# Kernel tuning notes

Measured on AMD Instinct MI355X. Metric: run time of the kernel, lower is better.

Reference implementation:

```python
import jax, jax.numpy as jnp
import numpy as np

N_EMBD = 1024
HEAD_SIZE = 128
B, T = 8, 4096


def setup_inputs() -> dict:
    key = jax.random.key(0)
    ks = jax.random.split(key, 7)
    s = 1.0 / np.sqrt(N_EMBD)
    return {
        "x": jax.random.normal(ks[0], (B, T, N_EMBD), dtype=jnp.float32),
        "Wq": jax.random.uniform(ks[1], (N_EMBD, HEAD_SIZE), jnp.float32, -s, s),
        "bq": jax.random.uniform(ks[2], (HEAD_SIZE,), jnp.float32, -s, s),
        "Wk": jax.random.uniform(ks[3], (N_EMBD, HEAD_SIZE), jnp.float32, -s, s),
        "bk": jax.random.uniform(ks[4], (HEAD_SIZE,), jnp.float32, -s, s),
        "Wv": jax.random.uniform(ks[5], (N_EMBD, HEAD_SIZE), jnp.float32, -s, s),
        "bv": jax.random.uniform(ks[6], (HEAD_SIZE,), jnp.float32, -s, s),
    }


def reference(x, Wq, bq, Wk, bk, Wv, bv):
    # q,k,v: [B,T,H]
    q = x @ Wq + bq
    k = x @ Wk + bk
    v = x @ Wv + bv
    scale = HEAD_SIZE ** -0.5
    att = jnp.einsum("bth,bsh->bts", q, k) * scale  # [B,T,T]
    t = x.shape[1]
    causal = jnp.tril(jnp.ones((t, t), dtype=bool))
    att = jnp.where(causal, att, -jnp.inf)
    att = jax.nn.softmax(att, axis=-1)
    # dropout with p=0.0 is identity (eval-mode equivalent)
    out = jnp.einsum("bts,bsh->bth", att, v)  # [B,T,H]
    return out
```

## Files before the change

### kernel.cpp

```cpp
#include <hip/hip_runtime.h>
#include <hip/hip_bf16.h>
#include <stdint.h>

#define BATCH 8
#define SEQ   4096
#define EMB   1024
#define HD    128
#define NROWS 32768

typedef __attribute__((ext_vector_type(8))) short short8;
typedef __attribute__((ext_vector_type(4))) float f32x4;

__device__ inline unsigned short f2bf(float f) {
    union { float f; unsigned int u; } c; c.f = f;
    unsigned int u = c.u;
    unsigned int r = (u + 0x7fffu + ((u >> 16) & 1u)) >> 16;
    return (unsigned short)r;
}
__device__ inline float bf2f(unsigned short u) {
    union { unsigned int i; float f; } c; c.i = ((unsigned int)u) << 16; return c.f;
}
__device__ inline unsigned int pkbf(float a, float b) {
    __hip_bfloat162 h = __float22bfloat162_rn(make_float2(a, b));
    union { __hip_bfloat162 h; unsigned int u; } c; c.h = h; return c.u;
}

#define GLDS16(gp, lp) __builtin_amdgcn_global_load_lds( \
    (const __attribute__((address_space(1))) void*)(gp), \
    (__attribute__((address_space(3))) void*)(lp), 16, 0, 0)

__global__ __launch_bounds__(256) void prep_kernel(
    const float* __restrict__ Wq, const float* __restrict__ bq,
    const float* __restrict__ Wk, const float* __restrict__ bk,
    const float* __restrict__ Wv, const float* __restrict__ bv,
    unsigned short* __restrict__ wt, float* __restrict__ biasc)
{
    const int n = blockIdx.x;
    const int sel = n >> 7, h = n & 127;
    const float* W = (sel == 0) ? Wq : (sel == 1) ? Wk : Wv;
    const int tid = threadIdx.x;
    const int k0 = tid * 4;
    union { unsigned short us[4]; uint2 v; } pk;
#pragma unroll
    for (int u = 0; u < 4; ++u) pk.us[u] = f2bf(W[(size_t)(k0 + u) * HD + h]);
    *(uint2*)&wt[(size_t)n * EMB + k0] = pk.v;
    if (tid == 0) {
        const float* bp = (sel == 0) ? bq : (sel == 1) ? bk : bv;
        biasc[n] = bp[h];
    }
}

__global__ __launch_bounds__(512, 4) void gemm_qkv(
    const float* __restrict__ x, const unsigned short* __restrict__ wt,
    const float* __restrict__ biasc,
    unsigned short* __restrict__ q, unsigned short* __restrict__ kOut,
    unsigned short* __restrict__ vt)
{
    const int m0  = blockIdx.x * 64;
    const int tid = threadIdx.x;
    const int wave = tid >> 6, lane = tid & 63;
    const int quad = lane >> 4, l15 = lane & 15;

    __shared__ __align__(16) unsigned short As[2][64][40];
    __shared__ __align__(16) unsigned short Bs[2][12288];

    f32x4 acc[3][4];
#pragma unroll
    for (int i = 0; i < 3; ++i)
#pragma unroll
        for (int j = 0; j < 4; ++j) acc[i][j] = (f32x4){0.f, 0.f, 0.f, 0.f};

    const int arow = tid >> 3, akc = (tid & 7) * 4;
    float4 aR;

#define LOAD_A(kt) aR = *(const float4*)(x + (size_t)(m0 + arow) * EMB + (kt) * 32 + akc);
#define WRITE_A(buf)                                                        \
    {                                                                       \
        union { unsigned short us[4]; uint2 v; } pw;                        \
        pw.us[0] = f2bf(aR.x); pw.us[1] = f2bf(aR.y);                       \
        pw.us[2] = f2bf(aR.z); pw.us[3] = f2bf(aR.w);                       \
        *(uint2*)&As[buf][arow][akc] = pw.v;                                \
    }
#define STAGE_B(kt, buf)                                                    \
    {                                                                       \
        _Pragma("unroll")                                                   \
        for (int g = 0; g < 3; ++g) {                                       \
            int s0 = (g * 8 + wave) * 64;                                   \
            int s  = s0 + lane;                                             \
            int n  = s >> 2, c = (s & 3) ^ (n & 3);                         \
            GLDS16(wt + (size_t)n * EMB + (kt) * 32 + c * 8,                \
                   &Bs[buf][s0 * 8]);                                       \
        }                                                                   \
    }

    LOAD_A(0); STAGE_B(0, 0); WRITE_A(0);
    int cur = 0;

    for (int kt = 0; kt < 32; ++kt) {
        __syncthreads();
        if (kt < 31) { LOAD_A(kt + 1); STAGE_B(kt + 1, cur ^ 1); }
        short8 af[4], bw[3];
#pragma unroll
        for (int mj = 0; mj < 4; ++mj)
            af[mj] = *(const short8*)&As[cur][mj * 16 + l15][quad * 8];
#pragma unroll
        for (int ni = 0; ni < 3; ++ni) {
            int n = wave * 48 + ni * 16 + l15;
            bw[ni] = *(const short8*)&Bs[cur][n * 32 + ((quad ^ (n & 3)) << 3)];
        }
#pragma unroll
        for (int ni = 0; ni < 3; ++ni)
#pragma unroll
            for (int mj = 0; mj < 4; ++mj)
                acc[ni][mj] = __builtin_amdgcn_mfma_f32_16x16x32_bf16(
                    bw[ni], af[mj], acc[ni][mj], 0, 0, 0);
        if (kt < 31) WRITE_A(cur ^ 1);
        cur ^= 1;
    }

    const float qscale = 0.08838834764831845f * 1.4426950408889634f;
    const int bb = m0 >> 12;
    const int t0 = m0 & 4095;
#pragma unroll
    for (int ni = 0; ni < 3; ++ni) {
        int colbase = wave * 48 + ni * 16;
        int sel = colbase >> 7;
        int c0 = colbase + quad * 4;
        float4 bv4 = *(const float4*)&biasc[c0];
#pragma unroll
        for (int mj = 0; mj < 4; ++mj) {
            int m = m0 + mj * 16 + l15;
            if (sel == 0) {
                union { unsigned short us[4]; uint2 v; } pk;
#pragma unroll
                for (int j = 0; j < 4; ++j)
                    pk.us[j] = f2bf((acc[ni][mj][j] + ((const float*)&bv4)[j]) * qscale);
                *(uint2*)&q[(size_t)m * HD + (c0 & 127)] = pk.v;
            } else if (sel == 1) {
                union { unsigned short us[4]; uint2 v; } pk;
#pragma unroll
                for (int j = 0; j < 4; ++j)
                    pk.us[j] = f2bf(acc[ni][mj][j] + ((const float*)&bv4)[j]);
                *(uint2*)&kOut[(size_t)m * HD + (c0 & 127)] = pk.v;
            } else {
#pragma unroll
                for (int j = 0; j < 4; ++j) {
                    int h = (c0 & 127) + j;
                    vt[((size_t)(bb * 128 + h)) * SEQ + t0 + mj * 16 + l15] =
                        f2bf(acc[ni][mj][j] + ((const float*)&bv4)[j]);
                }
            }
        }
    }
#undef LOAD_A
#undef WRITE_A
#undef STAGE_B
}

__global__ __launch_bounds__(512, 2) void attn_kernel(
    const unsigned short* __restrict__ q, const unsigned short* __restrict__ k,
    const unsigned short* __restrict__ vt, float* __restrict__ outA,
    unsigned short* __restrict__ Oh, float2* __restrict__ ml)
{
    const int rank   = blockIdx.x;
    const int qtA    = 31 - (rank >> 4);
    const int parity = (rank >> 3) & 1;
    const int b      = rank & 7;
    const int tid  = threadIdx.x;
    const int wave = tid >> 6, lane = tid & 63;
    const int quad = lane >> 4, l15 = lane & 15;
    const int qtW   = (wave < 4) ? qtA : (31 - qtA);
    const int qrow0 = qtW * 128 + (wave & 3) * 32;
    const size_t qbase = (size_t)b * SEQ;
    const size_t vbase = (size_t)b * HD * SEQ;

    __shared__ __align__(16) unsigned short Ks[2][8192];
    __shared__ __align__(16) unsigned short Vs[2][8192];

#define STAGE_KV(kt_, buf_)                                                  \
    {                                                                        \
        _Pragma("unroll")                                                    \
        for (int g = 0; g < 2; ++g) {                                        \
            int s0 = (g * 8 + wave) * 64;                                    \
            int s  = s0 + lane;                                              \
            int key = s >> 4, c = (s & 15) ^ (key & 15);                     \
            GLDS16(k + (qbase + (kt_) * 64 + key) * HD + c * 8,              \
                   &Ks[buf_][s0 * 8]);                                       \
        }                                                                    \
        _Pragma("unroll")                                                    \
        for (int g = 0; g < 2; ++g) {                                        \
            int s0 = (g * 8 + wave) * 64;                                    \
            int s  = s0 + lane;                                              \
            int h = s >> 3, c = (s & 7) ^ (h & 7);                           \
            GLDS16(vt + vbase + (size_t)h * SEQ + (kt_) * 64 + c * 8,        \
                   &Vs[buf_][s0 * 8]);                                       \
        }                                                                    \
    }

    short8 qf[2][4];
#pragma unroll
    for (int mi = 0; mi < 2; ++mi)
#pragma unroll
        for (int kh = 0; kh < 4; ++kh)
            qf[mi][kh] = *(const short8*)(q + (qbase + qrow0 + mi * 16 + l15) * HD + kh * 32 + quad * 8);

    f32x4 o[2][8];
#pragma unroll
    for (int mi = 0; mi < 2; ++mi)
#pragma unroll
        for (int hi = 0; hi < 8; ++hi) o[mi][hi] = (f32x4){0.f, 0.f, 0.f, 0.f};
    float m_r[2] = {-1e30f, -1e30f};
    float l_r[2] = {0.f, 0.f};

    const int bpa0 = (l15 + 16 * ((2 * quad) & 3)) * 4;
    const int bpa1 = (l15 + 16 * ((2 * quad + 1) & 3)) * 4;

    const int niter = qtA + 1;
    STAGE_KV(parity, 0);
    int cur = 0;

    for (int i = 0; i < niter; ++i) {
        const int kt = parity + 2 * i;
        const int key0 = kt * 64;
        __syncthreads();
        if (i + 1 < niter) STAGE_KV(kt + 2, cur ^ 1);

        if (i <= qtW) {
            f32x4 s[2][4];
#pragma unroll
            for (int mi = 0; mi < 2; ++mi)
#pragma unroll
                for (int ni = 0; ni < 4; ++ni) s[mi][ni] = (f32x4){0.f, 0.f, 0.f, 0.f};
#pragma unroll
            for (int kh = 0; kh < 4; ++kh) {
#pragma unroll
                for (int ni = 0; ni < 4; ++ni) {
                    short8 kf = *(const short8*)&Ks[cur][(ni * 16 + l15) * 128 + (((kh * 4 + quad) ^ l15) << 3)];
                    s[0][ni] = __builtin_amdgcn_mfma_f32_16x16x32_bf16(kf, qf[0][kh], s[0][ni], 0, 0, 0);
                    s[1][ni] = __builtin_amdgcn_mfma_f32_16x16x32_bf16(kf, qf[1][kh], s[1][ni], 0, 0, 0);
                }
            }
            if (key0 + 63 > qrow0) {
#pragma unroll
                for (int mi = 0; mi < 2; ++mi)
#pragma unroll
                    for (int ni = 0; ni < 4; ++ni)
#pragma unroll
                        for (int j = 0; j < 4; ++j) {
                            int key = key0 + ni * 16 + quad * 4 + j;
                            int t   = qrow0 + mi * 16 + l15;
                            if (key > t) s[mi][ni][j] = -1e30f;
                        }
            }
            unsigned int pk[2][4][2];
#pragma unroll
            for (int mi = 0; mi < 2; ++mi) {
                float mx = -1e30f;
#pragma unroll
                for (int ni = 0; ni < 4; ++ni)
#pragma unroll
                    for (int j = 0; j < 4; ++j) mx = fmaxf(mx, s[mi][ni][j]);
                mx = fmaxf(mx, __shfl_xor(mx, 16));
                mx = fmaxf(mx, __shfl_xor(mx, 32));
                float mnew = fmaxf(m_r[mi], mx);
                float alpha = __builtin_amdgcn_exp2f(m_r[mi] - mnew);
                m_r[mi] = mnew;
                float rs = 0.f;
#pragma unroll
                for (int ni = 0; ni < 4; ++ni) {
                    float p0 = __builtin_amdgcn_exp2f(s[mi][ni][0] - mnew);
                    float p1 = __builtin_amdgcn_exp2f(s[mi][ni][1] - mnew);
                    float p2 = __builtin_amdgcn_exp2f(s[mi][ni][2] - mnew);
                    float p3 = __builtin_amdgcn_exp2f(s[mi][ni][3] - mnew);
                    rs += (p0 + p1) + (p2 + p3);
                    pk[mi][ni][0] = pkbf(p0, p1);
                    pk[mi][ni][1] = pkbf(p2, p3);
                }
                rs += __shfl_xor(rs, 16);
                rs += __shfl_xor(rs, 32);
                l_r[mi] = alpha * l_r[mi] + rs;
#pragma unroll
                for (int hi = 0; hi < 8; ++hi) o[mi][hi] *= alpha;
            }
            short8 pT[2][2];
#pragma unroll
            for (int mi = 0; mi < 2; ++mi)
#pragma unroll
                for (int sk = 0; sk < 2; ++sk) {
                    union { unsigned int u[4]; short8 s8; } pt;
                    int lo = 2 * sk, hi_ = 2 * sk + 1;
                    unsigned int a0 = (unsigned)__builtin_amdgcn_ds_bpermute(bpa0, (int)pk[mi][lo][0]);
                    unsigned int b0 = (unsigned)__builtin_amdgcn_ds_bpermute(bpa0, (int)pk[mi][hi_][0]);
                    pt.u[0] = (quad < 2) ? a0 : b0;
                    unsigned int a1 = (unsigned)__builtin_amdgcn_ds_bpermute(bpa0, (int)pk[mi][lo][1]);
                    unsigned int b1 = (unsigned)__builtin_amdgcn_ds_bpermute(bpa0, (int)pk[mi][hi_][1]);
                    pt.u[1] = (quad < 2) ? a1 : b1;
                    unsigned int a2 = (unsigned)__builtin_amdgcn_ds_bpermute(bpa1, (int)pk[mi][lo][0]);
                    unsigned int b2 = (unsigned)__builtin_amdgcn_ds_bpermute(bpa1, (int)pk[mi][hi_][0]);
                    pt.u[2] = (quad < 2) ? a2 : b2;
                    unsigned int a3 = (unsigned)__builtin_amdgcn_ds_bpermute(bpa1, (int)pk[mi][lo][1]);
                    unsigned int b3 = (unsigned)__builtin_amdgcn_ds_bpermute(bpa1, (int)pk[mi][hi_][1]);
                    pt.u[3] = (quad < 2) ? a3 : b3;
                    pT[mi][sk] = pt.s8;
                }
#pragma unroll
            for (int sk = 0; sk < 2; ++sk)
#pragma unroll
                for (int hi = 0; hi < 8; ++hi) {
                    short8 vf = *(const short8*)&Vs[cur][(hi * 16 + l15) * 64 + (((sk * 4 + quad) ^ (l15 & 7)) << 3)];
                    o[0][hi] = __builtin_amdgcn_mfma_f32_16x16x32_bf16(vf, pT[0][sk], o[0][hi], 0, 0, 0);
                    o[1][hi] = __builtin_amdgcn_mfma_f32_16x16x32_bf16(vf, pT[1][sk], o[1][hi], 0, 0, 0);
                }
        }
        cur ^= 1;
    }

#pragma unroll
    for (int mi = 0; mi < 2; ++mi) {
        size_t rowg = qbase + qrow0 + mi * 16 + l15;
        if (quad == 0) ml[(size_t)parity * NROWS + rowg] = make_float2(m_r[mi], l_r[mi]);
#pragma unroll
        for (int hi = 0; hi < 8; ++hi) {
            if (parity == 0) {
                *(f32x4*)&outA[rowg * HD + hi * 16 + quad * 4] = o[mi][hi];
            } else {
                union { unsigned short us[4]; uint2 v; } pw;
#pragma unroll
                for (int j = 0; j < 4; ++j) pw.us[j] = f2bf(o[mi][hi][j]);
                *(uint2*)&Oh[rowg * HD + hi * 16 + quad * 4] = pw.v;
            }
        }
    }
#undef STAGE_KV
}

__global__ __launch_bounds__(256) void merge_kernel(
    float* __restrict__ out, const unsigned short* __restrict__ Oh,
    const float2* __restrict__ ml)
{
    int idx = blockIdx.x * 256 + threadIdx.x;
    int row = idx >> 5;
    int hc  = (idx & 31) << 2;
    float2 a = ml[row];
    float2 c = ml[NROWS + row];
    float M  = fmaxf(a.x, c.x);
    float w0 = __builtin_amdgcn_exp2f(a.x - M);
    float w1 = __builtin_amdgcn_exp2f(c.x - M);
    float inv = 1.0f / (w0 * a.y + w1 * c.y);
    f32x4 o0 = *(const f32x4*)&out[(size_t)row * HD + hc];
    union { unsigned short us[4]; uint2 v; } pv;
    pv.v = *(const uint2*)&Oh[(size_t)row * HD + hc];
    f32x4 r;
#pragma unroll
    for (int j = 0; j < 4; ++j)
        r[j] = (w0 * o0[j] + w1 * bf2f(pv.us[j])) * inv;
    *(f32x4*)&out[(size_t)row * HD + hc] = r;
}

extern "C" void kernel_launch(void* const* d_in, const int* in_sizes, int n_in,
                              void* d_out, int out_size, void* d_ws, size_t ws_size,
                              hipStream_t stream) {
    const float* x  = (const float*)d_in[0];
    const float* Wq = (const float*)d_in[1];
    const float* bq = (const float*)d_in[2];
    const float* Wk = (const float*)d_in[3];
    const float* bk = (const float*)d_in[4];
    const float* Wv = (const float*)d_in[5];
    const float* bv = (const float*)d_in[6];
    float* out = (float*)d_out;

    unsigned short* wt    = (unsigned short*)d_ws;
    float*          biasc = (float*)((char*)d_ws + 786432);
    unsigned short* qb    = (unsigned short*)((char*)d_ws + 787968);
    unsigned short* kb    = qb  + (size_t)NROWS * HD;
    unsigned short* vtb   = kb  + (size_t)NROWS * HD;
    unsigned short* Oh    = vtb + (size_t)NROWS * HD;
    float2*         ml    = (float2*)((char*)d_ws + 787968 + 4ull * NROWS * HD * 2);

    prep_kernel<<<dim3(384), 256, 0, stream>>>(Wq, bq, Wk, bk, Wv, bv, wt, biasc);
    gemm_qkv<<<dim3(512), 512, 0, stream>>>(x, wt, biasc, qb, kb, vtb);
    attn_kernel<<<dim3(256), 512, 0, stream>>>(qb, kb, vtb, out, Oh, ml);
    merge_kernel<<<dim3(NROWS * 32 / 256), 256, 0, stream>>>(out, Oh, ml);
}
```

Before: 320.4 us.

## Enlarge QKV GEMM tile to 128 rows with 12 waves per block

The QKV projection GEMM now computes a 128x384 tile per block using 12 waves arranged as 2 row groups by 6 column groups, each wave owning a 64x64 sub-tile. The grid is halved to 256 blocks. The aim is to reuse each staged weight tile across twice as many rows, cutting how often the weights are reloaded into shared memory and raising the MFMA-to-load ratio. In exchange it uses more LDS and registers per block and lowers occupancy, and only 512 of the 768 threads load A.

```diff
diff --git a/kernel.cpp b/kernel.cpp
--- a/kernel.cpp
+++ b/kernel.cpp
@@ -50,42 +50,52 @@
     }
 }
 
-__global__ __launch_bounds__(512, 4) void gemm_qkv(
+__global__ __launch_bounds__(768, 3) void gemm_qkv(
     const float* __restrict__ x, const unsigned short* __restrict__ wt,
     const float* __restrict__ biasc,
     unsigned short* __restrict__ q, unsigned short* __restrict__ kOut,
     unsigned short* __restrict__ vt)
 {
-    const int m0  = blockIdx.x * 64;
+    const int m0  = blockIdx.x * 128;
     const int tid = threadIdx.x;
     const int wave = tid >> 6, lane = tid & 63;
     const int quad = lane >> 4, l15 = lane & 15;
-
-    __shared__ __align__(16) unsigned short As[2][64][40];
+    const int wm = (wave >= 6) ? 1 : 0;
+    const int wn = wave - wm * 6;
+
+    __shared__ __align__(16) unsigned short As[2][128][40];
     __shared__ __align__(16) unsigned short Bs[2][12288];
 
-    f32x4 acc[3][4];
-#pragma unroll
-    for (int i = 0; i < 3; ++i)
+    f32x4 acc[4][4];
+#pragma unroll
+    for (int i = 0; i < 4; ++i)
 #pragma unroll
         for (int j = 0; j < 4; ++j) acc[i][j] = (f32x4){0.f, 0.f, 0.f, 0.f};
 
+    const int aactive = (tid < 512);
     const int arow = tid >> 3, akc = (tid & 7) * 4;
-    float4 aR;
-
-#define LOAD_A(kt) aR = *(const float4*)(x + (size_t)(m0 + arow) * EMB + (kt) * 32 + akc);
+    float4 aR0, aR1;
+
+#define LOAD_A(kt)                                                          \
+    if (aactive) {                                                          \
+        aR0 = *(const float4*)(x + (size_t)(m0 + arow) * EMB + (kt) * 32 + akc);        \
+        aR1 = *(const float4*)(x + (size_t)(m0 + arow + 64) * EMB + (kt) * 32 + akc);   \
+    }
 #define WRITE_A(buf)                                                        \
-    {                                                                       \
-        union { unsigned short us[4]; uint2 v; } pw;                        \
-        pw.us[0] = f2bf(aR.x); pw.us[1] = f2bf(aR.y);                       \
-        pw.us[2] = f2bf(aR.z); pw.us[3] = f2bf(aR.w);                       \
-        *(uint2*)&As[buf][arow][akc] = pw.v;                                \
+    if (aactive) {                                                          \
+        union { unsigned short us[4]; uint2 v; } p0, p1;                    \
+        p0.us[0] = f2bf(aR0.x); p0.us[1] = f2bf(aR0.y);                     \
+        p0.us[2] = f2bf(aR0.z); p0.us[3] = f2bf(aR0.w);                     \
+        *(uint2*)&As[buf][arow][akc] = p0.v;                                \
+        p1.us[0] = f2bf(aR1.x); p1.us[1] = f2bf(aR1.y);                     \
+        p1.us[2] = f2bf(aR1.z); p1.us[3] = f2bf(aR1.w);                     \
+        *(uint2*)&As[buf][arow + 64][akc] = p1.v;                           \
     }
 #define STAGE_B(kt, buf)                                                    \
     {                                                                       \
         _Pragma("unroll")                                                   \
-        for (int g = 0; g < 3; ++g) {                                       \
-            int s0 = (g * 8 + wave) * 64;                                   \
+        for (int g = 0; g < 2; ++g) {                                       \
+            int s0 = (g * 12 + wave) * 64;                                  \
             int s  = s0 + lane;                                             \
             int n  = s >> 2, c = (s & 3) ^ (n & 3);                         \
             GLDS16(wt + (size_t)n * EMB + (kt) * 32 + c * 8,                \
@@ -99,17 +109,17 @@
     for (int kt = 0; kt < 32; ++kt) {
         __syncthreads();
         if (kt < 31) { LOAD_A(kt + 1); STAGE_B(kt + 1, cur ^ 1); }
-        short8 af[4], bw[3];
+        short8 af[4], bw[4];
 #pragma unroll
         for (int mj = 0; mj < 4; ++mj)
-            af[mj] = *(const short8*)&As[cur][mj * 16 + l15][quad * 8];
-#pragma unroll
-        for (int ni = 0; ni < 3; ++ni) {
-            int n = wave * 48 + ni * 16 + l15;
+            af[mj] = *(const short8*)&As[cur][wm * 64 + mj * 16 + l15][quad * 8];
+#pragma unroll
+        for (int ni = 0; ni < 4; ++ni) {
+            int n = wn * 64 + ni * 16 + l15;
             bw[ni] = *(const short8*)&Bs[cur][n * 32 + ((quad ^ (n & 3)) << 3)];
         }
 #pragma unroll
-        for (int ni = 0; ni < 3; ++ni)
+        for (int ni = 0; ni < 4; ++ni)
 #pragma unroll
             for (int mj = 0; mj < 4; ++mj)
                 acc[ni][mj] = __builtin_amdgcn_mfma_f32_16x16x32_bf16(
@@ -121,15 +131,17 @@
     const float qscale = 0.08838834764831845f * 1.4426950408889634f;
     const int bb = m0 >> 12;
     const int t0 = m0 & 4095;
-#pragma unroll
-    for (int ni = 0; ni < 3; ++ni) {
-        int colbase = wave * 48 + ni * 16;
+    const int mrow0 = m0 + wm * 64;
+    const int tl0   = t0 + wm * 64;
+#pragma unroll
+    for (int ni = 0; ni < 4; ++ni) {
+        int colbase = wn * 64 + ni * 16;
         int sel = colbase >> 7;
         int c0 = colbase + quad * 4;
         float4 bv4 = *(const float4*)&biasc[c0];
 #pragma unroll
         for (int mj = 0; mj < 4; ++mj) {
-            int m = m0 + mj * 16 + l15;
+            int m = mrow0 + mj * 16 + l15;
             if (sel == 0) {
                 union { unsigned short us[4]; uint2 v; } pk;
 #pragma unroll
@@ -146,7 +158,7 @@
 #pragma unroll
                 for (int j = 0; j < 4; ++j) {
                     int h = (c0 & 127) + j;
-                    vt[((size_t)(bb * 128 + h)) * SEQ + t0 + mj * 16 + l15] =
+                    vt[((size_t)(bb * 128 + h)) * SEQ + tl0 + mj * 16 + l15] =
                         f2bf(acc[ni][mj][j] + ((const float*)&bv4)[j]);
                 }
             }
@@ -378,7 +390,7 @@
     float2*         ml    = (float2*)((char*)d_ws + 787968 + 4ull * NROWS * HD * 2);
 
     prep_kernel<<<dim3(384), 256, 0, stream>>>(Wq, bq, Wk, bk, Wv, bv, wt, biasc);
-    gemm_qkv<<<dim3(512), 512, 0, stream>>>(x, wt, biasc, qb, kb, vtb);
+    gemm_qkv<<<dim3(256), 768, 0, stream>>>(x, wt, biasc, qb, kb, vtb);
     attn_kernel<<<dim3(256), 512, 0, stream>>>(qb, kb, vtb, out, Oh, ml);
     merge_kernel<<<dim3(NROWS * 32 / 256), 256, 0, stream>>>(out, Oh, ml);
 }
```

After: 307.9 us. -3.9%, faster.
